# Optimization experiments

Measured on AMD Instinct MI355X. Metric: run time of the kernel, lower is better.

Reference implementation:

```python
import jax, jax.numpy as jnp
import numpy as np

B, C, H, W = 8, 320, 32, 32
HEADS, DHEAD = 8, 40
CTX_LEN, CTX_DIM = 77, 768
FF_INNER = 4 * C
GROUPS = 32
HW = H * W


def setup_inputs() -> dict:
    key = jax.random.key(0)
    ks = jax.random.split(key, 16)
    def nrm(k, shape, s=0.02):
        return (jax.random.normal(k, shape) * s).astype(jnp.float32)
    z = lambda *s: jnp.zeros(s, jnp.float32)
    o = lambda *s: jnp.ones(s, jnp.float32)
    inp = {}
    inp["x"] = jax.random.normal(ks[0], (B, C, H, W), jnp.float32)
    inp["context"] = jax.random.normal(ks[1], (B, CTX_LEN, CTX_DIM), jnp.float32)
    inp["vis_mask"] = jax.random.uniform(ks[2], (B, HW, HW)) > 0.5
    inp["v2t_mask"] = jax.random.uniform(ks[3], (B, HW, CTX_LEN)) > 0.5
    inp["gn_scale"] = o(C); inp["gn_bias"] = z(C)
    inp["proj_in_w"] = nrm(ks[4], (C, C)); inp["proj_in_b"] = z(C)
    inp["n1_s"] = o(C); inp["n1_b"] = z(C)
    inp["wq1"] = nrm(ks[5], (C, C)); inp["wk1"] = nrm(ks[6], (C, C)); inp["wv1"] = nrm(ks[7], (C, C))
    inp["wo1"] = nrm(ks[8], (C, C)); inp["bo1"] = z(C)
    inp["n2_s"] = o(C); inp["n2_b"] = z(C)
    inp["wq2"] = nrm(ks[9], (C, C)); inp["wk2"] = nrm(ks[10], (CTX_DIM, C)); inp["wv2"] = nrm(ks[11], (CTX_DIM, C))
    inp["wo2"] = nrm(ks[12], (C, C)); inp["bo2"] = z(C)
    inp["n3_s"] = o(C); inp["n3_b"] = z(C)
    inp["ff_w1"] = nrm(ks[13], (C, 2 * FF_INNER)); inp["ff_b1"] = z(2 * FF_INNER)
    inp["ff_w2"] = nrm(ks[14], (FF_INNER, C)); inp["ff_b2"] = z(C)
    inp["proj_out_w"] = nrm(ks[15], (C, C)); inp["proj_out_b"] = z(C)
    return inp


def group_norm(x, scale, bias, eps=1e-6):
    b, c, h, w = x.shape
    xg = x.reshape(b, GROUPS, -1)
    mu = xg.mean(-1, keepdims=True)
    var = xg.var(-1, keepdims=True)
    xn = ((xg - mu) * jax.lax.rsqrt(var + eps)).reshape(b, c, h, w)
    return xn * scale[None, :, None, None] + bias[None, :, None, None]


def layer_norm(x, s, b, eps=1e-5):
    mu = x.mean(-1, keepdims=True)
    var = x.var(-1, keepdims=True)
    return (x - mu) * jax.lax.rsqrt(var + eps) * s + b


def mha(xq, ctx, wq, wk, wv, wo, bo, mask):
    # CrossAttention: manual einsum softmax with boolean mask broadcast over heads
    b, n, _ = xq.shape
    m = ctx.shape[1]
    split = lambda t: t.reshape(b, -1, HEADS, DHEAD).transpose(0, 2, 1, 3)
    q = split(xq @ wq)   # [b,h,n,d]
    k = split(ctx @ wk)  # [b,h,m,d]
    v = split(ctx @ wv)
    sim = jnp.einsum('bhid,bhjd->bhij', q, k) * (DHEAD ** -0.5)
    if mask is not None:
        sim = jnp.where(mask[:, None, :, :], sim, jnp.finfo(sim.dtype).min)
    attn = jax.nn.softmax(sim, axis=-1)
    out = jnp.einsum('bhij,bhjd->bhid', attn, v)
    out = out.transpose(0, 2, 1, 3).reshape(b, n, HEADS * DHEAD)
    return out @ wo + bo


def reference(x, context, vis_mask, v2t_mask, gn_scale, gn_bias, proj_in_w, proj_in_b,
              n1_s, n1_b, wq1, wk1, wv1, wo1, bo1,
              n2_s, n2_b, wq2, wk2, wv2, wo2, bo2,
              n3_s, n3_b, ff_w1, ff_b1, ff_w2, ff_b2,
              proj_out_w, proj_out_b):
    x_in = x
    h = group_norm(x, gn_scale, gn_bias)
    # 1x1 conv proj_in == per-pixel linear; flatten b c h w -> b (hw) c
    h = h.reshape(B, C, HW).transpose(0, 2, 1) @ proj_in_w + proj_in_b
    # masked self-attention (vis mask)
    h = h + mha(layer_norm(h, n1_s, n1_b), layer_norm(h, n1_s, n1_b),
                wq1, wk1, wv1, wo1, bo1, vis_mask)
    # masked cross-attention to text (v2t mask)
    h = h + mha(layer_norm(h, n2_s, n2_b), context,
                wq2, wk2, wv2, wo2, bo2, v2t_mask)
    # GEGLU feedforward (glu=True, mult=4)
    y = layer_norm(h, n3_s, n3_b) @ ff_w1 + ff_b1
    a, g = jnp.split(y, 2, axis=-1)
    h = h + (a * jax.nn.gelu(g, approximate=False)) @ ff_w2 + ff_b2
    # proj_out + residual
    out = (h @ proj_out_w + proj_out_b).transpose(0, 2, 1).reshape(B, C, H, W)
    return out + x_in
```

## Files before the change

### kernel.cpp

```cpp
#include <hip/hip_runtime.h>
#include <hip/hip_bf16.h>
#include <math.h>


#define Bsz   8
#define Cch   320
#define HW    1024
#define NTOK  (Bsz*HW)
#define HEADS 8
#define DHEAD 40
#define CTXL  77
#define CTXD  768
#define FFI   1280
#define MCTX  (Bsz*CTXL)
#define MCTXP 640

typedef unsigned short u16;
typedef unsigned long long u64;
typedef __attribute__((ext_vector_type(8))) u16    u16x8;
typedef __attribute__((ext_vector_type(8))) __bf16 bf16x8;
typedef __attribute__((ext_vector_type(4))) float  f32x4;

__device__ inline u16 f2b(float f) {
    unsigned u = __float_as_uint(f);
    return (u16)((u + 0x7FFFu + ((u >> 16) & 1u)) >> 16);
}

__global__ __launch_bounds__(256) void gn_apply(
    const float* __restrict__ x, const float* __restrict__ gnA,
    const float* __restrict__ gnB, u16* __restrict__ out)
{
    __shared__ u16 T[64*72];
    const int tid = threadIdx.x;
    const int c0 = blockIdx.x * 64;
    const int p0 = blockIdx.y * 64;
    const int b  = blockIdx.z;
    for (int e = tid; e < 512; e += 256) {
        int r = e >> 3, ch = e & 7;
        const float* src = x + ((size_t)(b*Cch + c0 + r))*HW + p0 + ch*8;
        float a  = gnA[b*Cch + c0 + r];
        float bb = gnB[b*Cch + c0 + r];
        float4 v0 = *(const float4*)src;
        float4 v1 = *(const float4*)(src + 4);
        u16x8 val;
        val[0] = f2b(v0.x*a + bb); val[1] = f2b(v0.y*a + bb);
        val[2] = f2b(v0.z*a + bb); val[3] = f2b(v0.w*a + bb);
        val[4] = f2b(v1.x*a + bb); val[5] = f2b(v1.y*a + bb);
        val[6] = f2b(v1.z*a + bb); val[7] = f2b(v1.w*a + bb);
        *(u16x8*)&T[r*72 + (ch ^ (r & 7))*8] = val;
    }
    __syncthreads();
    for (int e = tid; e < 4096; e += 256) {
        int p = e >> 6, c = e & 63;
        u16 v = T[c*72 + (((p >> 3) ^ (c & 7))*8) + (p & 7)];
        out[((size_t)(b*HW + p0 + p))*Cch + c0 + c] = v;
    }
}

__global__ __launch_bounds__(256) void layernorm_kernel(
    const float* __restrict__ in, const float* __restrict__ s,
    const float* __restrict__ bgain, u16* __restrict__ out)
{
    int t = blockIdx.x*4 + (threadIdx.x >> 6);
    int lane = threadIdx.x & 63;
    const float* row = in + (size_t)t*Cch;
    float v[5];
    float sum = 0.f, sq = 0.f;
    #pragma unroll
    for (int i = 0; i < 5; ++i) {
        v[i] = row[lane + 64*i];
        sum += v[i]; sq += v[i]*v[i];
    }
    #pragma unroll
    for (int off = 32; off > 0; off >>= 1) {
        sum += __shfl_xor(sum, off);
        sq  += __shfl_xor(sq,  off);
    }
    float mean = sum * (1.f/320.f);
    float var  = sq  * (1.f/320.f) - mean*mean;
    float inv  = rsqrtf(var + 1e-5f);
    u16* orow = out + (size_t)t*Cch;
    #pragma unroll
    for (int i = 0; i < 5; ++i) {
        int c = lane + 64*i;
        orow[c] = f2b((v[i]-mean)*inv*s[c] + bgain[c]);
    }
}

struct WDesc { const float* src; u16* dst; int K; int N; int tiles; float scl; };
struct WPack { WDesc w[12]; };

#define WT_TILES 620
#define CTXBLK   240

__global__ __launch_bounds__(256) void preamble(
    WPack p, const float* __restrict__ ctxsrc, u16* __restrict__ ctxdst,
    const void* __restrict__ vis, const void* __restrict__ v2t,
    u64* __restrict__ bvis, u64* __restrict__ bv2t,
    const float* __restrict__ x, const float* __restrict__ gscale,
    const float* __restrict__ gbias, float* __restrict__ gnA,
    float* __restrict__ gnB)
{
    __shared__ u16 T[64*72];
    int blk = blockIdx.x;
    int tid = threadIdx.x;
    if (blk < WT_TILES) {
        int t = blk;
        #pragma unroll
        for (int i = 0; i < 12; ++i) {
            int nt = p.w[i].tiles;
            if (t < nt) {
                const int K = p.w[i].K, N = p.w[i].N;
                const int ntN = N >> 6;
                const int tk = t / ntN, tn = t - tk*ntN;
                const float scl = p.w[i].scl;
                const float* src = p.w[i].src;
                u16* dst = p.w[i].dst;
                for (int e = tid; e < 512; e += 256) {
                    int r = e >> 3, ch = e & 7;
                    const float* sp = src + (size_t)(tk*64 + r)*N + tn*64 + ch*8;
                    float4 v0 = *(const float4*)sp;
                    float4 v1 = *(const float4*)(sp + 4);
                    u16x8 val;
                    val[0] = f2b(v0.x*scl); val[1] = f2b(v0.y*scl);
                    val[2] = f2b(v0.z*scl); val[3] = f2b(v0.w*scl);
                    val[4] = f2b(v1.x*scl); val[5] = f2b(v1.y*scl);
                    val[6] = f2b(v1.z*scl); val[7] = f2b(v1.w*scl);
                    *(u16x8*)&T[r*72 + (ch ^ (r & 7))*8] = val;
                }
                __syncthreads();
                for (int e = tid; e < 4096; e += 256) {
                    int n = e >> 6, k = e & 63;
                    u16 v = T[k*72 + (((n >> 3) ^ (k & 7))*8) + (n & 7)];
                    dst[(size_t)(tn*64 + n)*K + tk*64 + k] = v;
                }
                return;
            }
            t -= nt;
        }
        return;
    }
    if (blk < WT_TILES + CTXBLK) {
        int idx = (blk - WT_TILES)*2048 + tid*8;
        int r = idx / CTXD;
        u16x8 val = {};
        if (r < MCTX) {
            float4 v0 = *(const float4*)(ctxsrc + idx);
            float4 v1 = *(const float4*)(ctxsrc + idx + 4);
            val[0] = f2b(v0.x); val[1] = f2b(v0.y);
            val[2] = f2b(v0.z); val[3] = f2b(v0.w);
            val[4] = f2b(v1.x); val[5] = f2b(v1.y);
            val[6] = f2b(v1.z); val[7] = f2b(v1.w);
        }
        *(u16x8*)(ctxdst + idx) = val;
        return;
    }
    if (blk >= WT_TILES + CTXBLK + 4096) {
        int gb = blk - (WT_TILES + CTXBLK + 4096);
        int b = gb >> 5, g = gb & 31;
        __shared__ float rs[256], rq[256];
        const float4* xg = (const float4*)(x + ((size_t)b*Cch + g*10)*HW);
        float s = 0.f, q = 0.f;
        #pragma unroll
        for (int i = 0; i < 10; ++i) {
            float4 v = xg[tid + i*256];
            s += v.x + v.y + v.z + v.w;
            q += v.x*v.x + v.y*v.y + v.z*v.z + v.w*v.w;
        }
        rs[tid] = s; rq[tid] = q; __syncthreads();
        for (int off = 128; off > 0; off >>= 1) {
            if (tid < off) { rs[tid] += rs[tid+off]; rq[tid] += rq[tid+off]; }
            __syncthreads();
        }
        if (tid < 10) {
            float mean = rs[0] * (1.f/10240.f);
            float var  = rq[0] * (1.f/10240.f) - mean*mean;
            float inv  = rsqrtf(var + 1e-6f);
            int chn = g*10 + tid;
            float a = inv * gscale[chn];
            gnA[b*Cch + chn] = a;
            gnB[b*Cch + chn] = gbias[chn] - mean*a;
        }
        return;
    }
    __shared__ int any;
    if (tid == 0) any = 0;
    __syncthreads();
    const unsigned char* probe = (const unsigned char*)vis;
    for (int i = tid; i < 4096; i += 256)
        if ((i & 3) && probe[i]) any = 1;
    __syncthreads();
    const int isU8 = any;
    int mb = blk - WT_TILES - CTXBLK;
    const void* mask; u64* bits; int Lkv, nw;
    if (mb < 2048) { mask = vis; bits = bvis; Lkv = HW;   nw = 16; }
    else           { mask = v2t; bits = bv2t; Lkv = CTXL; nw = 2; mb -= 2048; }
    const int wv = tid >> 6, lane = tid & 63;
    const int row = mb*4 + wv;
    const unsigned char* m8  = (const unsigned char*)mask;
    const int*           m32 = (const int*)mask;
    const size_t base = (size_t)row * Lkv;
    for (int w = 0; w < nw; ++w) {
        int j = w*64 + lane;
        bool on = (j < Lkv) && (isU8 ? (m8[base+j] != 0) : (m32[base+j] != 0));
        u64 word = __ballot(on);
        if (lane == 0) bits[(size_t)row*nw + w] = word;
    }
}

__global__ __launch_bounds__(512) void gemm_bf16(
    const u16* __restrict__ A, const u16* __restrict__ Wt,
    const float* __restrict__ bias, const float* __restrict__ res,
    float* __restrict__ out, u16* __restrict__ out_bf, int M, int N, int K)
{
    __shared__ u16 As[2][128*40];
    __shared__ u16 Bs[2][64*40];
    const int tid  = threadIdx.x;
    const int lane = tid & 63;
    const int w    = tid >> 6;
    const int mp   = w >> 1;
    const int np   = w & 1;
    const int m0   = blockIdx.y * 128;
    const int n0   = blockIdx.x * 64;
    const int fr   = lane & 15, fg = lane >> 4;
    const int ar   = tid >> 2, ac = tid & 3;
    const bool hasB = tid < 256;

    const u16* pa = A  + (size_t)(m0 + ar)*K + ac*8;
    const u16* pb = Wt + (size_t)(n0 + ar)*K + ac*8;
    const int nk = K >> 5;

    *(u16x8*)&As[0][ar*40 + ac*8] = *(const u16x8*)pa;
    if (hasB) *(u16x8*)&Bs[0][ar*40 + ac*8] = *(const u16x8*)pb;
    u16x8 xa = *(const u16x8*)(pa + 32);
    u16x8 ya = *(const u16x8*)(pa + 64);
    u16x8 xb = {}, yb = {};
    if (hasB) { xb = *(const u16x8*)(pb + 32); yb = *(const u16x8*)(pb + 64); }

    f32x4 acc[2][2] = {};
    for (int i = 0; i < nk; i += 2) {
        __syncthreads();
        *(u16x8*)&As[1][ar*40 + ac*8] = xa;
        if (hasB) *(u16x8*)&Bs[1][ar*40 + ac*8] = xb;
        if (i + 3 < nk) {
            xa = *(const u16x8*)(pa + 32*(i+3));
            if (hasB) xb = *(const u16x8*)(pb + 32*(i+3));
        }
        {
            bf16x8 a0 = *(const bf16x8*)&As[0][(mp*32      + fr)*40 + fg*8];
            bf16x8 a1 = *(const bf16x8*)&As[0][(mp*32 + 16 + fr)*40 + fg*8];
            #pragma unroll
            for (int t = 0; t < 2; ++t) {
                bf16x8 b = *(const bf16x8*)&Bs[0][((np*2+t)*16 + fr)*40 + fg*8];
                acc[0][t] = __builtin_amdgcn_mfma_f32_16x16x32_bf16(a0, b, acc[0][t], 0, 0, 0);
                acc[1][t] = __builtin_amdgcn_mfma_f32_16x16x32_bf16(a1, b, acc[1][t], 0, 0, 0);
            }
        }
        __syncthreads();
        if (i + 2 < nk) {
            *(u16x8*)&As[0][ar*40 + ac*8] = ya;
            if (hasB) *(u16x8*)&Bs[0][ar*40 + ac*8] = yb;
            if (i + 4 < nk) {
                ya = *(const u16x8*)(pa + 32*(i+4));
                if (hasB) yb = *(const u16x8*)(pb + 32*(i+4));
            }
        }
        {
            bf16x8 a0 = *(const bf16x8*)&As[1][(mp*32      + fr)*40 + fg*8];
            bf16x8 a1 = *(const bf16x8*)&As[1][(mp*32 + 16 + fr)*40 + fg*8];
            #pragma unroll
            for (int t = 0; t < 2; ++t) {
                bf16x8 b = *(const bf16x8*)&Bs[1][((np*2+t)*16 + fr)*40 + fg*8];
                acc[0][t] = __builtin_amdgcn_mfma_f32_16x16x32_bf16(a0, b, acc[0][t], 0, 0, 0);
                acc[1][t] = __builtin_amdgcn_mfma_f32_16x16x32_bf16(a1, b, acc[1][t], 0, 0, 0);
            }
        }
    }
    #pragma unroll
    for (int at = 0; at < 2; ++at) {
        #pragma unroll
        for (int t = 0; t < 2; ++t) {
            int gn = n0 + (np*2+t)*16 + fr;
            float bv = bias ? bias[gn] : 0.f;
            #pragma unroll
            for (int i = 0; i < 4; ++i) {
                int gm = m0 + mp*32 + at*16 + fg*4 + i;
                float v = acc[at][t][i] + bv;
                if (res) v += res[(size_t)gm*N + gn];
                if (out) out[(size_t)gm*N + gn] = v;
                if (out_bf) out_bf[(size_t)gm*N + gn] = f2b(v);
            }
        }
    }
}

__global__ __launch_bounds__(512) void gemm_pout(
    const u16* __restrict__ A, const u16* __restrict__ Wt,
    const float* __restrict__ bias, const float* __restrict__ x,
    float* __restrict__ out, int K)
{
    __shared__ u16 As[2][128*40];
    __shared__ u16 Bs[2][64*40];
    const int tid  = threadIdx.x;
    const int lane = tid & 63;
    const int w    = tid >> 6;
    const int mp   = w >> 1;
    const int np   = w & 1;
    const int m0   = blockIdx.y * 128;
    const int n0   = blockIdx.x * 64;
    const int fr   = lane & 15, fg = lane >> 4;
    const int ar   = tid >> 2, ac = tid & 3;
    const bool hasB = tid < 256;

    const u16* pa = A  + (size_t)(m0 + ar)*K + ac*8;
    const u16* pb = Wt + (size_t)(n0 + ar)*K + ac*8;
    const int nk = K >> 5;

    *(u16x8*)&As[0][ar*40 + ac*8] = *(const u16x8*)pa;
    if (hasB) *(u16x8*)&Bs[0][ar*40 + ac*8] = *(const u16x8*)pb;
    u16x8 xa = *(const u16x8*)(pa + 32);
    u16x8 ya = *(const u16x8*)(pa + 64);
    u16x8 xb = {}, yb = {};
    if (hasB) { xb = *(const u16x8*)(pb + 32); yb = *(const u16x8*)(pb + 64); }

    f32x4 acc[2][2] = {};
    for (int i = 0; i < nk; i += 2) {
        __syncthreads();
        *(u16x8*)&As[1][ar*40 + ac*8] = xa;
        if (hasB) *(u16x8*)&Bs[1][ar*40 + ac*8] = xb;
        if (i + 3 < nk) {
            xa = *(const u16x8*)(pa + 32*(i+3));
            if (hasB) xb = *(const u16x8*)(pb + 32*(i+3));
        }
        {
            bf16x8 a0 = *(const bf16x8*)&As[0][(mp*32      + fr)*40 + fg*8];
            bf16x8 a1 = *(const bf16x8*)&As[0][(mp*32 + 16 + fr)*40 + fg*8];
            #pragma unroll
            for (int t = 0; t < 2; ++t) {
                bf16x8 b = *(const bf16x8*)&Bs[0][((np*2+t)*16 + fr)*40 + fg*8];
                acc[0][t] = __builtin_amdgcn_mfma_f32_16x16x32_bf16(a0, b, acc[0][t], 0, 0, 0);
                acc[1][t] = __builtin_amdgcn_mfma_f32_16x16x32_bf16(a1, b, acc[1][t], 0, 0, 0);
            }
        }
        __syncthreads();
        if (i + 2 < nk) {
            *(u16x8*)&As[0][ar*40 + ac*8] = ya;
            if (hasB) *(u16x8*)&Bs[0][ar*40 + ac*8] = yb;
            if (i + 4 < nk) {
                ya = *(const u16x8*)(pa + 32*(i+4));
                if (hasB) yb = *(const u16x8*)(pb + 32*(i+4));
            }
        }
        {
            bf16x8 a0 = *(const bf16x8*)&As[1][(mp*32      + fr)*40 + fg*8];
            bf16x8 a1 = *(const bf16x8*)&As[1][(mp*32 + 16 + fr)*40 + fg*8];
            #pragma unroll
            for (int t = 0; t < 2; ++t) {
                bf16x8 b = *(const bf16x8*)&Bs[1][((np*2+t)*16 + fr)*40 + fg*8];
                acc[0][t] = __builtin_amdgcn_mfma_f32_16x16x32_bf16(a0, b, acc[0][t], 0, 0, 0);
                acc[1][t] = __builtin_amdgcn_mfma_f32_16x16x32_bf16(a1, b, acc[1][t], 0, 0, 0);
            }
        }
    }
    #pragma unroll
    for (int at = 0; at < 2; ++at) {
        #pragma unroll
        for (int t = 0; t < 2; ++t) {
            int gn = n0 + (np*2+t)*16 + fr;
            float bv = bias[gn];
            int gm0 = m0 + mp*32 + at*16 + fg*4;
            int b   = gm0 >> 10;
            int pcol= gm0 & (HW-1);
            size_t o = ((size_t)(b*Cch + gn))*HW + pcol;
            f32x4 xv = *(const f32x4*)&x[o];
            f32x4 vv;
            #pragma unroll
            for (int i = 0; i < 4; ++i) vv[i] = acc[at][t][i] + bv + xv[i];
            *(f32x4*)&out[o] = vv;
        }
    }
}

__global__ __launch_bounds__(512) void ctx_kv_gemm(
    const u16* __restrict__ ctx, const u16* __restrict__ wk,
    const u16* __restrict__ wv, u16* __restrict__ kout, u16* __restrict__ vout)
{
    __shared__ u16 As[2][64*40];
    __shared__ u16 Bs[2][64*40];
    const int tid  = threadIdx.x;
    const int lane = tid & 63;
    const int w    = tid >> 6;
    const int mg   = w >> 1;
    const int np   = w & 1;
    const int m0   = blockIdx.y * 64;
    const int n0   = blockIdx.x * 64;
    const u16* Wt  = blockIdx.z ? wv : wk;
    u16* outp      = blockIdx.z ? vout : kout;
    const int fr   = lane & 15, fg = lane >> 4;
    const bool isA = tid < 256;
    const int cr   = (tid & 255) >> 2, cc = tid & 3;

    const u16* ps = isA ? ctx + (size_t)(m0 + cr)*CTXD + cc*8
                        : Wt  + (size_t)(n0 + cr)*CTXD + cc*8;
    u16* s0 = isA ? &As[0][cr*40 + cc*8] : &Bs[0][cr*40 + cc*8];
    u16* s1 = isA ? &As[1][cr*40 + cc*8] : &Bs[1][cr*40 + cc*8];
    const int nk = CTXD >> 5;

    *(u16x8*)s0 = *(const u16x8*)ps;
    u16x8 xv = *(const u16x8*)(ps + 32);
    u16x8 yv = *(const u16x8*)(ps + 64);

    f32x4 acc[2] = {};
    for (int i = 0; i < nk; i += 2) {
        __syncthreads();
        *(u16x8*)s1 = xv;
        if (i + 3 < nk) xv = *(const u16x8*)(ps + 32*(i+3));
        {
            bf16x8 a = *(const bf16x8*)&As[0][(mg*16 + fr)*40 + fg*8];
            #pragma unroll
            for (int t = 0; t < 2; ++t) {
                bf16x8 b = *(const bf16x8*)&Bs[0][((np*2+t)*16 + fr)*40 + fg*8];
                acc[t] = __builtin_amdgcn_mfma_f32_16x16x32_bf16(a, b, acc[t], 0, 0, 0);
            }
        }
        __syncthreads();
        if (i + 2 < nk) {
            *(u16x8*)s0 = yv;
            if (i + 4 < nk) yv = *(const u16x8*)(ps + 32*(i+4));
        }
        {
            bf16x8 a = *(const bf16x8*)&As[1][(mg*16 + fr)*40 + fg*8];
            #pragma unroll
            for (int t = 0; t < 2; ++t) {
                bf16x8 b = *(const bf16x8*)&Bs[1][((np*2+t)*16 + fr)*40 + fg*8];
                acc[t] = __builtin_amdgcn_mfma_f32_16x16x32_bf16(a, b, acc[t], 0, 0, 0);
            }
        }
    }
    #pragma unroll
    for (int t = 0; t < 2; ++t) {
        int gn = n0 + (np*2+t)*16 + fr;
        #pragma unroll
        for (int i = 0; i < 4; ++i) {
            int gm = m0 + mg*16 + fg*4 + i;
            if (gm < MCTX)
                outp[(size_t)gm*Cch + gn] = f2b(acc[t][i]);
        }
    }
}

__global__ __launch_bounds__(512) void geglu_bf16(
    const u16* __restrict__ A, const u16* __restrict__ Wt,
    const float* __restrict__ b1, u16* __restrict__ out, int M, int K)
{
    __shared__ u16 As[2][128*40];
    __shared__ u16 Ba[2][64*40];
    __shared__ u16 Bg[2][64*40];
    const int tid  = threadIdx.x;
    const int lane = tid & 63;
    const int w    = tid >> 6;
    const int mp   = w >> 1;
    const int np   = w & 1;
    const int m0   = blockIdx.y * 128;
    const int n0   = blockIdx.x * 64;
    const int fr   = lane & 15, fg = lane >> 4;
    const int ar   = tid >> 2, ac = tid & 3;
    const int nk   = K >> 5;

    const u16* pa = A + (size_t)(m0 + ar)*K + ac*8;
    const int bq = (ar < 64) ? (n0 + ar) : (FFI + n0 + ar - 64);
    const u16* pb = Wt + (size_t)bq*K + ac*8;
    u16* bs0 = (ar < 64) ? &Ba[0][ar*40 + ac*8] : &Bg[0][(ar-64)*40 + ac*8];
    u16* bs1 = (ar < 64) ? &Ba[1][ar*40 + ac*8] : &Bg[1][(ar-64)*40 + ac*8];

    *(u16x8*)&As[0][ar*40 + ac*8] = *(const u16x8*)pa;
    *(u16x8*)bs0 = *(const u16x8*)pb;
    u16x8 xa = *(const u16x8*)(pa + 32);
    u16x8 xb = *(const u16x8*)(pb + 32);
    u16x8 ya = *(const u16x8*)(pa + 64);
    u16x8 yb = *(const u16x8*)(pb + 64);

    f32x4 aca[2][2] = {}, acg[2][2] = {};
    for (int i = 0; i < nk; i += 2) {
        __syncthreads();
        *(u16x8*)&As[1][ar*40 + ac*8] = xa;
        *(u16x8*)bs1 = xb;
        if (i + 3 < nk) {
            xa = *(const u16x8*)(pa + 32*(i+3));
            xb = *(const u16x8*)(pb + 32*(i+3));
        }
        {
            bf16x8 a0 = *(const bf16x8*)&As[0][(mp*32      + fr)*40 + fg*8];
            bf16x8 a1 = *(const bf16x8*)&As[0][(mp*32 + 16 + fr)*40 + fg*8];
            #pragma unroll
            for (int t = 0; t < 2; ++t) {
                bf16x8 ba = *(const bf16x8*)&Ba[0][((np*2+t)*16 + fr)*40 + fg*8];
                bf16x8 bg = *(const bf16x8*)&Bg[0][((np*2+t)*16 + fr)*40 + fg*8];
                aca[0][t] = __builtin_amdgcn_mfma_f32_16x16x32_bf16(a0, ba, aca[0][t], 0, 0, 0);
                aca[1][t] = __builtin_amdgcn_mfma_f32_16x16x32_bf16(a1, ba, aca[1][t], 0, 0, 0);
                acg[0][t] = __builtin_amdgcn_mfma_f32_16x16x32_bf16(a0, bg, acg[0][t], 0, 0, 0);
                acg[1][t] = __builtin_amdgcn_mfma_f32_16x16x32_bf16(a1, bg, acg[1][t], 0, 0, 0);
            }
        }
        __syncthreads();
        if (i + 2 < nk) {
            *(u16x8*)&As[0][ar*40 + ac*8] = ya;
            *(u16x8*)bs0 = yb;
            if (i + 4 < nk) {
                ya = *(const u16x8*)(pa + 32*(i+4));
                yb = *(const u16x8*)(pb + 32*(i+4));
            }
        }
        {
            bf16x8 a0 = *(const bf16x8*)&As[1][(mp*32      + fr)*40 + fg*8];
            bf16x8 a1 = *(const bf16x8*)&As[1][(mp*32 + 16 + fr)*40 + fg*8];
            #pragma unroll
            for (int t = 0; t < 2; ++t) {
                bf16x8 ba = *(const bf16x8*)&Ba[1][((np*2+t)*16 + fr)*40 + fg*8];
                bf16x8 bg = *(const bf16x8*)&Bg[1][((np*2+t)*16 + fr)*40 + fg*8];
                aca[0][t] = __builtin_amdgcn_mfma_f32_16x16x32_bf16(a0, ba, aca[0][t], 0, 0, 0);
                aca[1][t] = __builtin_amdgcn_mfma_f32_16x16x32_bf16(a1, ba, aca[1][t], 0, 0, 0);
                acg[0][t] = __builtin_amdgcn_mfma_f32_16x16x32_bf16(a0, bg, acg[0][t], 0, 0, 0);
                acg[1][t] = __builtin_amdgcn_mfma_f32_16x16x32_bf16(a1, bg, acg[1][t], 0, 0, 0);
            }
        }
    }
    #pragma unroll
    for (int at = 0; at < 2; ++at) {
        #pragma unroll
        for (int t = 0; t < 2; ++t) {
            int gn = n0 + (np*2+t)*16 + fr;
            float ba = b1[gn], bg = b1[FFI + gn];
            #pragma unroll
            for (int i = 0; i < 4; ++i) {
                int gm = m0 + mp*32 + at*16 + fg*4 + i;
                float av = aca[at][t][i] + ba;
                float gv = acg[at][t][i] + bg;
                float gel = 0.5f*gv*(1.f + erff(gv*0.70710678118654752f));
                out[(size_t)gm*FFI + gn] = f2b(av*gel);
            }
        }
    }
}

__global__ __launch_bounds__(256) void transpose_v(
    const u16* __restrict__ in, int istride, u16* __restrict__ out,
    int Ltok, int ostride)
{
    __shared__ u16 T[64*72];
    const int tid = threadIdx.x;
    const int c0 = blockIdx.x * 64;
    const int t0 = blockIdx.y * 64;
    const int b  = blockIdx.z;
    for (int e = tid; e < 512; e += 256) {
        int r = e >> 3, ch = e & 7;
        u16x8 val = {};
        if (t0 + r < Ltok)
            val = *(const u16x8*)(in + ((size_t)(b*Ltok + t0 + r))*istride + c0 + ch*8);
        *(u16x8*)&T[r*72 + (ch ^ (r & 7))*8] = val;
    }
    __syncthreads();
    for (int e = tid; e < 4096; e += 256) {
        int c = e >> 6, t = e & 63;
        u16 v = T[t*72 + (((c >> 3) ^ (t & 7))*8) + (c & 7)];
        out[((size_t)(b*Cch + c0 + c))*ostride + t0 + t] = v;
    }
}

__global__ __launch_bounds__(512) void flash_mfma(
    const u16* __restrict__ qb, int qstride,
    const u16* __restrict__ kb, int kstride,
    const u16* __restrict__ vt, int vstride,
    const u64* __restrict__ mbits, int nw,
    u16* __restrict__ out,
    int Lkv)
{
    __shared__ u16 QPs[128*72];
    __shared__ u16 Ks[2][64*72];
    __shared__ u16 Vs[2][48*72];

    const int tid  = threadIdx.x;
    const int lane = tid & 63;
    const int w    = tid >> 6;
    const int col  = lane & 15;
    const int quad = lane >> 4;
    const int bi   = blockIdx.x;
    const int hb   = (bi & 7)*8 + (bi >> 6);
    const int qt   = (bi >> 3) & 7;
    const int h    = hb & 7;
    const int b    = hb >> 3;
    const int q0   = qt*128;
    const int ch   = tid & 7;
    const int r0   = tid >> 3;

    {
        const u16* qT = qb + ((size_t)(b*HW + q0))*qstride + (size_t)h*DHEAD + ch*8;
        u16x8 v0 = {}, v1 = {};
        if (ch < 5) {
            v0 = *(const u16x8*)(qT + (size_t)r0*qstride);
            v1 = *(const u16x8*)(qT + (size_t)(r0+64)*qstride);
        }
        *(u16x8*)&QPs[r0*72 + ch*8]      = v0;
        *(u16x8*)&QPs[(r0+64)*72 + ch*8] = v1;
    }
    if (tid < 128) {
        int rr  = tid >> 3;
        int row = 40 + (rr & 7);
        int buf = rr >> 3;
        u16x8 v = {};
        if (row == DHEAD) {
            #pragma unroll
            for (int z = 0; z < 8; ++z) v[z] = 0x3F80;
        }
        *(u16x8*)&Vs[buf][row*72 + ch*8] = v;
    }

    const bool kok = ch < 5;
    const u16* kR = kb + (size_t)b*Lkv*kstride + (size_t)h*DHEAD + ch*8
                       + (size_t)r0*kstride;
    const u16* vR = vt + ((size_t)(b*Cch + h*DHEAD))*vstride + ch*8
                       + (size_t)r0*vstride;
    const bool vok = r0 < DHEAD;
    const u64* mrow = mbits + ((size_t)(b*HW + q0 + w*16 + quad*4))*nw;

    u16x8 nk = {}, nv = {};
    if (kok && r0 < Lkv) nk = *(const u16x8*)kR;
    if (vok) nv = *(const u16x8*)vR;

    __syncthreads();
    const bf16x8 qa0 = *(const bf16x8*)&QPs[(w*16 + col)*72 +  0 + quad*8];
    const bf16x8 qa1 = *(const bf16x8*)&QPs[(w*16 + col)*72 + 32 + quad*8];

    f32x4 acc_o[3] = {};

    const int nkt = (Lkv + 63) / 64;
    int cur = 0;
    for (int jt = 0; jt < nkt; ++jt) {
        *(u16x8*)&Ks[cur][r0*72 + ch*8] = nk;
        if (vok) *(u16x8*)&Vs[cur][r0*72 + ch*8] = nv;
        if (jt + 1 < nkt) {
            kR += (size_t)64*kstride;
            vR += 64;
            nk = (u16x8){};
            if (kok && ((jt+1)*64 + r0 < Lkv)) nk = *(const u16x8*)kR;
            if (vok) nv = *(const u16x8*)vR;
        }
        __syncthreads();

        u64 mw[4];
        #pragma unroll
        for (int i = 0; i < 4; ++i) mw[i] = mrow[i*nw + jt];

        f32x4 s[4] = {};
        #pragma unroll
        for (int nt = 0; nt < 4; ++nt) {
            bf16x8 b0 = *(const bf16x8*)&Ks[cur][(nt*16 + col)*72 +  0 + quad*8];
            bf16x8 b1 = *(const bf16x8*)&Ks[cur][(nt*16 + col)*72 + 32 + quad*8];
            s[nt] = __builtin_amdgcn_mfma_f32_16x16x32_bf16(qa0, b0, s[nt], 0, 0, 0);
            s[nt] = __builtin_amdgcn_mfma_f32_16x16x32_bf16(qa1, b1, s[nt], 0, 0, 0);
        }

        #pragma unroll
        for (int i = 0; i < 4; ++i) {
            #pragma unroll
            for (int nt = 0; nt < 4; ++nt) {
                float p = __builtin_amdgcn_exp2f(s[nt][i]);
                unsigned bits = (unsigned)(mw[i] >> (nt*16));
                s[nt][i] = ((bits >> col) & 1u) ? p : 0.f;
            }
        }

        #pragma unroll
        for (int nt = 0; nt < 4; ++nt)
            #pragma unroll
            for (int i = 0; i < 4; ++i)
                QPs[(w*16 + quad*4 + i)*68 + nt*16 + col] =
                    (u16)(__float_as_uint(s[nt][i]) >> 16);

        bf16x8 pa0, pa1;
        __builtin_memcpy(&pa0, &QPs[(w*16 + col)*68 +  0 + quad*8], 16);
        __builtin_memcpy(&pa1, &QPs[(w*16 + col)*68 + 32 + quad*8], 16);
        #pragma unroll
        for (int nt = 0; nt < 3; ++nt) {
            bf16x8 vb0 = *(const bf16x8*)&Vs[cur][(nt*16 + col)*72 +  0 + quad*8];
            bf16x8 vb1 = *(const bf16x8*)&Vs[cur][(nt*16 + col)*72 + 32 + quad*8];
            acc_o[nt] = __builtin_amdgcn_mfma_f32_16x16x32_bf16(pa0, vb0, acc_o[nt], 0, 0, 0);
            acc_o[nt] = __builtin_amdgcn_mfma_f32_16x16x32_bf16(pa1, vb1, acc_o[nt], 0, 0, 0);
        }
        cur ^= 1;
    }

    float inv_l[4];
    #pragma unroll
    for (int i = 0; i < 4; ++i)
        inv_l[i] = 1.f / __shfl(acc_o[2][i], (lane & 48) | 8);

    #pragma unroll
    for (int nt = 0; nt < 3; ++nt) {
        int d = nt*16 + col;
        if (d < DHEAD) {
            #pragma unroll
            for (int i = 0; i < 4; ++i) {
                int q = q0 + w*16 + quad*4 + i;
                out[((size_t)(b*HW + q))*Cch + h*DHEAD + d] = f2b(acc_o[nt][i] * inv_l[i]);
            }
        }
    }
}

extern "C" void kernel_launch(void* const* d_in, const int* in_sizes, int n_in,
                              void* d_out, int out_size, void* d_ws, size_t ws_size,
                              hipStream_t stream)
{
    const float* x        = (const float*)d_in[0];
    const float* context  = (const float*)d_in[1];
    const void*  vis_mask = d_in[2];
    const void*  v2t_mask = d_in[3];
    const float* gn_s     = (const float*)d_in[4];
    const float* gn_b     = (const float*)d_in[5];
    const float* proj_in_w= (const float*)d_in[6];
    const float* proj_in_b= (const float*)d_in[7];
    const float* n1_s     = (const float*)d_in[8];
    const float* n1_b     = (const float*)d_in[9];
    const float* wq1      = (const float*)d_in[10];
    const float* wk1      = (const float*)d_in[11];
    const float* wv1      = (const float*)d_in[12];
    const float* wo1      = (const float*)d_in[13];
    const float* bo1      = (const float*)d_in[14];
    const float* n2_s     = (const float*)d_in[15];
    const float* n2_b     = (const float*)d_in[16];
    const float* wq2      = (const float*)d_in[17];
    const float* wk2      = (const float*)d_in[18];
    const float* wv2      = (const float*)d_in[19];
    const float* wo2      = (const float*)d_in[20];
    const float* bo2      = (const float*)d_in[21];
    const float* n3_s     = (const float*)d_in[22];
    const float* n3_b     = (const float*)d_in[23];
    const float* ff_w1    = (const float*)d_in[24];
    const float* ff_b1    = (const float*)d_in[25];
    const float* ff_w2    = (const float*)d_in[26];
    const float* ff_b2    = (const float*)d_in[27];
    const float* pout_w   = (const float*)d_in[28];
    const float* pout_b   = (const float*)d_in[29];
    float* out = (float*)d_out;

    const size_t TOKC = (size_t)NTOK*Cch;
    float* ws   = (float*)d_ws;
    float* Hb   = ws;
    u16*   QKV  = (u16*)(Hb + TOKC);
    u16*   Vt_g = QKV + 3*TOKC;
    u16*   G_bf = QKV;
    u16*   T0b  = Vt_g + TOKC;
    u16*   T1b  = T0b + TOKC;
    u16*   Hb_bf= T1b + TOKC;
    u16*   Wbf  = Hb_bf + TOKC;
    u64*   mb_vis = (u64*)(Wbf + 2539520);
    u64*   mb_v2t = mb_vis + 131072;
    u16*   ctx_bf = (u16*)(mb_v2t + 16384);
    u16*   Kc_bf  = ctx_bf + MCTXP*CTXD;
    u16*   Vc_bf  = Kc_bf + 640*Cch;
    float* gnA    = (float*)(Vc_bf + 640*Cch);
    float* gnB    = gnA + Bsz*Cch;

    u16* w_q1  = Wbf;
    u16* w_k1  = Wbf +  102400;
    u16* w_v1  = Wbf +  204800;
    u16* w_pin = Wbf +  307200;
    u16* w_o1  = Wbf +  409600;
    u16* w_q2  = Wbf +  512000;
    u16* w_o2  = Wbf +  614400;
    u16* w_ff1 = Wbf +  716800;
    u16* w_ff2 = Wbf + 1536000;
    u16* w_po  = Wbf + 1945600;
    u16* w_k2  = Wbf + 2048000;
    u16* w_v2  = Wbf + 2293760;

    const float qscale = 0.15811388300841897f * 1.4426950408889634f;
    WPack pack;
    pack.w[0]  = { wq1,       w_q1,  Cch, Cch, 25,  qscale };
    pack.w[1]  = { wk1,       w_k1,  Cch, Cch, 25,  1.f };
    pack.w[2]  = { wv1,       w_v1,  Cch, Cch, 25,  1.f };
    pack.w[3]  = { proj_in_w, w_pin, Cch, Cch, 25,  1.f };
    pack.w[4]  = { wo1,       w_o1,  Cch, Cch, 25,  1.f };
    pack.w[5]  = { wq2,       w_q2,  Cch, Cch, 25,  qscale };
    pack.w[6]  = { wo2,       w_o2,  Cch, Cch, 25,  1.f };
    pack.w[7]  = { ff_w1,     w_ff1, Cch, 2*FFI, 200, 1.f };
    pack.w[8]  = { ff_w2,     w_ff2, FFI, Cch, 100, 1.f };
    pack.w[9]  = { pout_w,    w_po,  Cch, Cch, 25,  1.f };
    pack.w[10] = { wk2,       w_k2,  CTXD, Cch, 60, 1.f };
    pack.w[11] = { wv2,       w_v2,  CTXD, Cch, 60, 1.f };

    dim3 blk256(256);
    dim3 blk512(512);
    dim3 gTok(Cch/64, NTOK/128);
    dim3 gQKV(960/64, NTOK/128);
    dim3 gKV(Cch/64, MCTXP/64, 2);
    dim3 gFF(FFI/64, NTOK/128);
    dim3 gTrS(Cch/64, HW/64, Bsz);
    dim3 gTrX(Cch/64, 2, Bsz);
    dim3 gGN(Cch/64, HW/64, Bsz);

    preamble<<<WT_TILES + CTXBLK + 4096 + 256, blk256, 0, stream>>>(
        pack, context, ctx_bf, vis_mask, v2t_mask, mb_vis, mb_v2t,
        x, gn_s, gn_b, gnA, gnB);

    gn_apply<<<gGN, blk256, 0, stream>>>(x, gnA, gnB, T0b);
    gemm_bf16<<<gTok, blk512, 0, stream>>>(T0b, w_pin, proj_in_b, nullptr, Hb, nullptr, NTOK, Cch, Cch);

    layernorm_kernel<<<NTOK/4, blk256, 0, stream>>>(Hb, n1_s, n1_b, T0b);
    gemm_bf16<<<gQKV, blk512, 0, stream>>>(T0b, w_q1, nullptr, nullptr, nullptr, QKV, NTOK, 960, Cch);
    transpose_v<<<gTrS, blk256, 0, stream>>>(QKV + 640, 960, Vt_g, HW, HW);
    flash_mfma<<<512, blk512, 0, stream>>>(QKV, 960, QKV + 320, 960, Vt_g, HW,
                                           mb_vis, 16, T1b, HW);
    gemm_bf16<<<gTok, blk512, 0, stream>>>(T1b, w_o1, bo1, Hb, Hb, nullptr, NTOK, Cch, Cch);

    layernorm_kernel<<<NTOK/4, blk256, 0, stream>>>(Hb, n2_s, n2_b, T0b);
    gemm_bf16<<<gTok, blk512, 0, stream>>>(T0b, w_q2, nullptr, nullptr, nullptr, QKV, NTOK, Cch, Cch);
    ctx_kv_gemm<<<gKV, blk512, 0, stream>>>(ctx_bf, w_k2, w_v2, Kc_bf, Vc_bf);
    transpose_v<<<gTrX, blk256, 0, stream>>>(Vc_bf, Cch, Vt_g, CTXL, 128);
    flash_mfma<<<512, blk512, 0, stream>>>(QKV, Cch, Kc_bf, Cch, Vt_g, 128,
                                           mb_v2t, 2, T1b, CTXL);
    gemm_bf16<<<gTok, blk512, 0, stream>>>(T1b, w_o2, bo2, Hb, Hb, nullptr, NTOK, Cch, Cch);

    layernorm_kernel<<<NTOK/4, blk256, 0, stream>>>(Hb, n3_s, n3_b, T0b);
    geglu_bf16<<<gFF, blk512, 0, stream>>>(T0b, w_ff1, ff_b1, G_bf, NTOK, Cch);
    gemm_bf16<<<gTok, blk512, 0, stream>>>(G_bf, w_ff2, ff_b2, Hb, nullptr, Hb_bf, NTOK, Cch, FFI);

    gemm_pout<<<gTok, blk512, 0, stream>>>(Hb_bf, w_po, pout_b, x, out, Cch);
}
```

Baseline: 375.9 us.

## Fuse LayerNorm into GEMM prologues and merge context KV and transposes

Removes the standalone layernorm kernels. Each consuming GEMM (QKV, Q2, GEGLU) now computes per-row mean and variance from the fp32 residual and normalises while staging A tiles to bf16. The context K/V GEMM now runs as extra blocks of the first QKV launch, and the two V transposes are merged into one launch, which cuts launch count and the bf16 round trip through global memory. The trade-off is that every N-tile block re-reads the fp32 rows to compute statistics, so A-side traffic is duplicated across column tiles. The fused blocks also carry extra register pressure.

```diff
diff --git a/kernel.cpp b/kernel.cpp
--- a/kernel.cpp
+++ b/kernel.cpp
@@ -54,36 +54,6 @@
         int p = e >> 6, c = e & 63;
         u16 v = T[c*72 + (((p >> 3) ^ (c & 7))*8) + (p & 7)];
         out[((size_t)(b*HW + p0 + p))*Cch + c0 + c] = v;
-    }
-}
-
-__global__ __launch_bounds__(256) void layernorm_kernel(
-    const float* __restrict__ in, const float* __restrict__ s,
-    const float* __restrict__ bgain, u16* __restrict__ out)
-{
-    int t = blockIdx.x*4 + (threadIdx.x >> 6);
-    int lane = threadIdx.x & 63;
-    const float* row = in + (size_t)t*Cch;
-    float v[5];
-    float sum = 0.f, sq = 0.f;
-    #pragma unroll
-    for (int i = 0; i < 5; ++i) {
-        v[i] = row[lane + 64*i];
-        sum += v[i]; sq += v[i]*v[i];
-    }
-    #pragma unroll
-    for (int off = 32; off > 0; off >>= 1) {
-        sum += __shfl_xor(sum, off);
-        sq  += __shfl_xor(sq,  off);
-    }
-    float mean = sum * (1.f/320.f);
-    float var  = sq  * (1.f/320.f) - mean*mean;
-    float inv  = rsqrtf(var + 1e-5f);
-    u16* orow = out + (size_t)t*Cch;
-    #pragma unroll
-    for (int i = 0; i < 5; ++i) {
-        int c = lane + 64*i;
-        orow[c] = f2b((v[i]-mean)*inv*s[c] + bgain[c]);
     }
 }
 
@@ -294,6 +264,194 @@
     }
 }
 
+__global__ __launch_bounds__(512) void gemm_ln(
+    const float* __restrict__ Af, const float* __restrict__ lns,
+    const float* __restrict__ lnb, const u16* __restrict__ Wt,
+    u16* __restrict__ out_bf, int N, int nqkv,
+    const u16* __restrict__ ctx, const u16* __restrict__ wk,
+    const u16* __restrict__ wv, u16* __restrict__ kout, u16* __restrict__ vout)
+{
+    __shared__ u16 As[2][128*40];
+    __shared__ u16 Bs[2][64*40];
+    const int tid  = threadIdx.x;
+    const int lane = tid & 63;
+    const int w    = tid >> 6;
+    const int fr   = lane & 15, fg = lane >> 4;
+    const int bi   = blockIdx.x;
+
+    if (bi < nqkv) {
+        const int K  = Cch;
+        const int nx = N >> 6;
+        const int n0 = (bi % nx)*64;
+        const int m0 = (bi / nx)*128;
+        const int mp = w >> 1, np = w & 1;
+        const int ar = tid >> 2, ac = tid & 3;
+        const bool hasB = tid < 256;
+
+        const float* rowp = Af + (size_t)(m0 + ar)*K;
+        float mean, inv;
+        {
+            const float* pp = rowp + ac*80;
+            float sum = 0.f, sq = 0.f;
+            #pragma unroll
+            for (int i = 0; i < 20; ++i) {
+                float4 v = *(const float4*)(pp + i*4);
+                sum += v.x+v.y+v.z+v.w;
+                sq  += v.x*v.x+v.y*v.y+v.z*v.z+v.w*v.w;
+            }
+            sum += __shfl_xor(sum, 1); sq += __shfl_xor(sq, 1);
+            sum += __shfl_xor(sum, 2); sq += __shfl_xor(sq, 2);
+            mean = sum * (1.f/320.f);
+            inv  = rsqrtf(sq * (1.f/320.f) - mean*mean + 1e-5f);
+        }
+
+        const float* paf = rowp + ac*8;
+        const u16*   pb  = Wt + (size_t)(n0 + ar)*K + ac*8;
+        const int nk = K >> 5;
+
+        #define LNPACK(v0, v1, c) ({                                        \
+            float4 s0_ = *(const float4*)(lns+(c)), s1_ = *(const float4*)(lns+(c)+4); \
+            float4 g0_ = *(const float4*)(lnb+(c)), g1_ = *(const float4*)(lnb+(c)+4); \
+            u16x8 r_;                                                       \
+            r_[0]=f2b(((v0).x-mean)*inv*s0_.x+g0_.x);                       \
+            r_[1]=f2b(((v0).y-mean)*inv*s0_.y+g0_.y);                       \
+            r_[2]=f2b(((v0).z-mean)*inv*s0_.z+g0_.z);                       \
+            r_[3]=f2b(((v0).w-mean)*inv*s0_.w+g0_.w);                       \
+            r_[4]=f2b(((v1).x-mean)*inv*s1_.x+g1_.x);                       \
+            r_[5]=f2b(((v1).y-mean)*inv*s1_.y+g1_.y);                       \
+            r_[6]=f2b(((v1).z-mean)*inv*s1_.z+g1_.z);                       \
+            r_[7]=f2b(((v1).w-mean)*inv*s1_.w+g1_.w);                       \
+            r_; })
+
+        {
+            float4 v0 = *(const float4*)paf, v1 = *(const float4*)(paf+4);
+            *(u16x8*)&As[0][ar*40 + ac*8] = LNPACK(v0, v1, ac*8);
+        }
+        if (hasB) *(u16x8*)&Bs[0][ar*40 + ac*8] = *(const u16x8*)pb;
+        float4 xa0 = *(const float4*)(paf+32), xa1 = *(const float4*)(paf+36);
+        float4 ya0 = *(const float4*)(paf+64), ya1 = *(const float4*)(paf+68);
+        u16x8 xb = {}, yb = {};
+        if (hasB) { xb = *(const u16x8*)(pb+32); yb = *(const u16x8*)(pb+64); }
+
+        f32x4 acc[2][2] = {};
+        for (int i = 0; i < nk; i += 2) {
+            __syncthreads();
+            *(u16x8*)&As[1][ar*40 + ac*8] = LNPACK(xa0, xa1, (i+1)*32 + ac*8);
+            if (hasB) *(u16x8*)&Bs[1][ar*40 + ac*8] = xb;
+            if (i + 3 < nk) {
+                xa0 = *(const float4*)(paf + 32*(i+3));
+                xa1 = *(const float4*)(paf + 32*(i+3) + 4);
+                if (hasB) xb = *(const u16x8*)(pb + 32*(i+3));
+            }
+            {
+                bf16x8 a0 = *(const bf16x8*)&As[0][(mp*32      + fr)*40 + fg*8];
+                bf16x8 a1 = *(const bf16x8*)&As[0][(mp*32 + 16 + fr)*40 + fg*8];
+                #pragma unroll
+                for (int t = 0; t < 2; ++t) {
+                    bf16x8 b = *(const bf16x8*)&Bs[0][((np*2+t)*16 + fr)*40 + fg*8];
+                    acc[0][t] = __builtin_amdgcn_mfma_f32_16x16x32_bf16(a0, b, acc[0][t], 0, 0, 0);
+                    acc[1][t] = __builtin_amdgcn_mfma_f32_16x16x32_bf16(a1, b, acc[1][t], 0, 0, 0);
+                }
+            }
+            __syncthreads();
+            if (i + 2 < nk) {
+                *(u16x8*)&As[0][ar*40 + ac*8] = LNPACK(ya0, ya1, (i+2)*32 + ac*8);
+                if (hasB) *(u16x8*)&Bs[0][ar*40 + ac*8] = yb;
+                if (i + 4 < nk) {
+                    ya0 = *(const float4*)(paf + 32*(i+4));
+                    ya1 = *(const float4*)(paf + 32*(i+4) + 4);
+                    if (hasB) yb = *(const u16x8*)(pb + 32*(i+4));
+                }
+            }
+            {
+                bf16x8 a0 = *(const bf16x8*)&As[1][(mp*32      + fr)*40 + fg*8];
+                bf16x8 a1 = *(const bf16x8*)&As[1][(mp*32 + 16 + fr)*40 + fg*8];
+                #pragma unroll
+                for (int t = 0; t < 2; ++t) {
+                    bf16x8 b = *(const bf16x8*)&Bs[1][((np*2+t)*16 + fr)*40 + fg*8];
+                    acc[0][t] = __builtin_amdgcn_mfma_f32_16x16x32_bf16(a0, b, acc[0][t], 0, 0, 0);
+                    acc[1][t] = __builtin_amdgcn_mfma_f32_16x16x32_bf16(a1, b, acc[1][t], 0, 0, 0);
+                }
+            }
+        }
+        #undef LNPACK
+        #pragma unroll
+        for (int at = 0; at < 2; ++at) {
+            #pragma unroll
+            for (int t = 0; t < 2; ++t) {
+                int gn = n0 + (np*2+t)*16 + fr;
+                #pragma unroll
+                for (int i = 0; i < 4; ++i) {
+                    int gm = m0 + mp*32 + at*16 + fg*4 + i;
+                    out_bf[(size_t)gm*N + gn] = f2b(acc[at][t][i]);
+                }
+            }
+        }
+        return;
+    }
+
+    {
+        int cb = bi - nqkv;
+        const int z  = cb / 50; cb -= z*50;
+        const int my = cb / 5, nx0 = cb - my*5;
+        const int m0 = my*64, n0 = nx0*64;
+        const u16* Wt2 = z ? wv : wk;
+        u16* outp      = z ? vout : kout;
+        const int mg = w >> 1;
+        const int np = w & 1;
+        const bool isA = tid < 256;
+        const int cr = (tid & 255) >> 2, cc = tid & 3;
+
+        const u16* ps = isA ? ctx + (size_t)(m0 + cr)*CTXD + cc*8
+                            : Wt2 + (size_t)(n0 + cr)*CTXD + cc*8;
+        u16* s0 = isA ? &As[0][cr*40 + cc*8] : &Bs[0][cr*40 + cc*8];
+        u16* s1 = isA ? &As[1][cr*40 + cc*8] : &Bs[1][cr*40 + cc*8];
+        const int nk = CTXD >> 5;
+
+        *(u16x8*)s0 = *(const u16x8*)ps;
+        u16x8 xv = *(const u16x8*)(ps + 32);
+        u16x8 yv = *(const u16x8*)(ps + 64);
+
+        f32x4 acc[2] = {};
+        for (int i = 0; i < nk; i += 2) {
+            __syncthreads();
+            *(u16x8*)s1 = xv;
+            if (i + 3 < nk) xv = *(const u16x8*)(ps + 32*(i+3));
+            {
+                bf16x8 a = *(const bf16x8*)&As[0][(mg*16 + fr)*40 + fg*8];
+                #pragma unroll
+                for (int t = 0; t < 2; ++t) {
+                    bf16x8 b = *(const bf16x8*)&Bs[0][((np*2+t)*16 + fr)*40 + fg*8];
+                    acc[t] = __builtin_amdgcn_mfma_f32_16x16x32_bf16(a, b, acc[t], 0, 0, 0);
+                }
+            }
+            __syncthreads();
+            if (i + 2 < nk) {
+                *(u16x8*)s0 = yv;
+                if (i + 4 < nk) yv = *(const u16x8*)(ps + 32*(i+4));
+            }
+            {
+                bf16x8 a = *(const bf16x8*)&As[1][(mg*16 + fr)*40 + fg*8];
+                #pragma unroll
+                for (int t = 0; t < 2; ++t) {
+                    bf16x8 b = *(const bf16x8*)&Bs[1][((np*2+t)*16 + fr)*40 + fg*8];
+                    acc[t] = __builtin_amdgcn_mfma_f32_16x16x32_bf16(a, b, acc[t], 0, 0, 0);
+                }
+            }
+        }
+        #pragma unroll
+        for (int t = 0; t < 2; ++t) {
+            int gn = n0 + (np*2+t)*16 + fr;
+            #pragma unroll
+            for (int i = 0; i < 4; ++i) {
+                int gm = m0 + mg*16 + fg*4 + i;
+                if (gm < MCTX)
+                    outp[(size_t)gm*Cch + gn] = f2b(acc[t][i]);
+            }
+        }
+    }
+}
+
 __global__ __launch_bounds__(512) void gemm_pout(
     const u16* __restrict__ A, const u16* __restrict__ Wt,
     const float* __restrict__ bias, const float* __restrict__ x,
@@ -381,77 +539,10 @@
     }
 }
 
-__global__ __launch_bounds__(512) void ctx_kv_gemm(
-    const u16* __restrict__ ctx, const u16* __restrict__ wk,
-    const u16* __restrict__ wv, u16* __restrict__ kout, u16* __restrict__ vout)
-{
-    __shared__ u16 As[2][64*40];
-    __shared__ u16 Bs[2][64*40];
-    const int tid  = threadIdx.x;
-    const int lane = tid & 63;
-    const int w    = tid >> 6;
-    const int mg   = w >> 1;
-    const int np   = w & 1;
-    const int m0   = blockIdx.y * 64;
-    const int n0   = blockIdx.x * 64;
-    const u16* Wt  = blockIdx.z ? wv : wk;
-    u16* outp      = blockIdx.z ? vout : kout;
-    const int fr   = lane & 15, fg = lane >> 4;
-    const bool isA = tid < 256;
-    const int cr   = (tid & 255) >> 2, cc = tid & 3;
-
-    const u16* ps = isA ? ctx + (size_t)(m0 + cr)*CTXD + cc*8
-                        : Wt  + (size_t)(n0 + cr)*CTXD + cc*8;
-    u16* s0 = isA ? &As[0][cr*40 + cc*8] : &Bs[0][cr*40 + cc*8];
-    u16* s1 = isA ? &As[1][cr*40 + cc*8] : &Bs[1][cr*40 + cc*8];
-    const int nk = CTXD >> 5;
-
-    *(u16x8*)s0 = *(const u16x8*)ps;
-    u16x8 xv = *(const u16x8*)(ps + 32);
-    u16x8 yv = *(const u16x8*)(ps + 64);
-
-    f32x4 acc[2] = {};
-    for (int i = 0; i < nk; i += 2) {
-        __syncthreads();
-        *(u16x8*)s1 = xv;
-        if (i + 3 < nk) xv = *(const u16x8*)(ps + 32*(i+3));
-        {
-            bf16x8 a = *(const bf16x8*)&As[0][(mg*16 + fr)*40 + fg*8];
-            #pragma unroll
-            for (int t = 0; t < 2; ++t) {
-                bf16x8 b = *(const bf16x8*)&Bs[0][((np*2+t)*16 + fr)*40 + fg*8];
-                acc[t] = __builtin_amdgcn_mfma_f32_16x16x32_bf16(a, b, acc[t], 0, 0, 0);
-            }
-        }
-        __syncthreads();
-        if (i + 2 < nk) {
-            *(u16x8*)s0 = yv;
-            if (i + 4 < nk) yv = *(const u16x8*)(ps + 32*(i+4));
-        }
-        {
-            bf16x8 a = *(const bf16x8*)&As[1][(mg*16 + fr)*40 + fg*8];
-            #pragma unroll
-            for (int t = 0; t < 2; ++t) {
-                bf16x8 b = *(const bf16x8*)&Bs[1][((np*2+t)*16 + fr)*40 + fg*8];
-                acc[t] = __builtin_amdgcn_mfma_f32_16x16x32_bf16(a, b, acc[t], 0, 0, 0);
-            }
-        }
-    }
-    #pragma unroll
-    for (int t = 0; t < 2; ++t) {
-        int gn = n0 + (np*2+t)*16 + fr;
-        #pragma unroll
-        for (int i = 0; i < 4; ++i) {
-            int gm = m0 + mg*16 + fg*4 + i;
-            if (gm < MCTX)
-                outp[(size_t)gm*Cch + gn] = f2b(acc[t][i]);
-        }
-    }
-}
-
-__global__ __launch_bounds__(512) void geglu_bf16(
-    const u16* __restrict__ A, const u16* __restrict__ Wt,
-    const float* __restrict__ b1, u16* __restrict__ out, int M, int K)
+__global__ __launch_bounds__(512) void geglu_ln(
+    const float* __restrict__ Af, const float* __restrict__ lns,
+    const float* __restrict__ lnb, const u16* __restrict__ Wt,
+    const float* __restrict__ b1, u16* __restrict__ out)
 {
     __shared__ u16 As[2][128*40];
     __shared__ u16 Ba[2][64*40];
@@ -465,29 +556,65 @@
     const int n0   = blockIdx.x * 64;
     const int fr   = lane & 15, fg = lane >> 4;
     const int ar   = tid >> 2, ac = tid & 3;
+    const int K    = Cch;
     const int nk   = K >> 5;
 
-    const u16* pa = A + (size_t)(m0 + ar)*K + ac*8;
+    const float* rowp = Af + (size_t)(m0 + ar)*K;
+    float mean, inv;
+    {
+        const float* pp = rowp + ac*80;
+        float sum = 0.f, sq = 0.f;
+        #pragma unroll
+        for (int i = 0; i < 20; ++i) {
+            float4 v = *(const float4*)(pp + i*4);
+            sum += v.x+v.y+v.z+v.w;
+            sq  += v.x*v.x+v.y*v.y+v.z*v.z+v.w*v.w;
+        }
+        sum += __shfl_xor(sum, 1); sq += __shfl_xor(sq, 1);
+        sum += __shfl_xor(sum, 2); sq += __shfl_xor(sq, 2);
+        mean = sum * (1.f/320.f);
+        inv  = rsqrtf(sq * (1.f/320.f) - mean*mean + 1e-5f);
+    }
+
+    const float* paf = rowp + ac*8;
     const int bq = (ar < 64) ? (n0 + ar) : (FFI + n0 + ar - 64);
     const u16* pb = Wt + (size_t)bq*K + ac*8;
     u16* bs0 = (ar < 64) ? &Ba[0][ar*40 + ac*8] : &Bg[0][(ar-64)*40 + ac*8];
     u16* bs1 = (ar < 64) ? &Ba[1][ar*40 + ac*8] : &Bg[1][(ar-64)*40 + ac*8];
 
-    *(u16x8*)&As[0][ar*40 + ac*8] = *(const u16x8*)pa;
+    #define LNPACK(v0, v1, c) ({                                            \
+        float4 s0_ = *(const float4*)(lns+(c)), s1_ = *(const float4*)(lns+(c)+4); \
+        float4 g0_ = *(const float4*)(lnb+(c)), g1_ = *(const float4*)(lnb+(c)+4); \
+        u16x8 r_;                                                           \
+        r_[0]=f2b(((v0).x-mean)*inv*s0_.x+g0_.x);                           \
+        r_[1]=f2b(((v0).y-mean)*inv*s0_.y+g0_.y);                           \
+        r_[2]=f2b(((v0).z-mean)*inv*s0_.z+g0_.z);                           \
+        r_[3]=f2b(((v0).w-mean)*inv*s0_.w+g0_.w);                           \
+        r_[4]=f2b(((v1).x-mean)*inv*s1_.x+g1_.x);                           \
+        r_[5]=f2b(((v1).y-mean)*inv*s1_.y+g1_.y);                           \
+        r_[6]=f2b(((v1).z-mean)*inv*s1_.z+g1_.z);                           \
+        r_[7]=f2b(((v1).w-mean)*inv*s1_.w+g1_.w);                           \
+        r_; })
+
+    {
+        float4 v0 = *(const float4*)paf, v1 = *(const float4*)(paf+4);
+        *(u16x8*)&As[0][ar*40 + ac*8] = LNPACK(v0, v1, ac*8);
+    }
     *(u16x8*)bs0 = *(const u16x8*)pb;
-    u16x8 xa = *(const u16x8*)(pa + 32);
+    float4 xa0 = *(const float4*)(paf+32), xa1 = *(const float4*)(paf+36);
+    float4 ya0 = *(const float4*)(paf+64), ya1 = *(const float4*)(paf+68);
     u16x8 xb = *(const u16x8*)(pb + 32);
-    u16x8 ya = *(const u16x8*)(pa + 64);
     u16x8 yb = *(const u16x8*)(pb + 64);
 
     f32x4 aca[2][2] = {}, acg[2][2] = {};
     for (int i = 0; i < nk; i += 2) {
         __syncthreads();
-        *(u16x8*)&As[1][ar*40 + ac*8] = xa;
+        *(u16x8*)&As[1][ar*40 + ac*8] = LNPACK(xa0, xa1, (i+1)*32 + ac*8);
         *(u16x8*)bs1 = xb;
         if (i + 3 < nk) {
-            xa = *(const u16x8*)(pa + 32*(i+3));
-            xb = *(const u16x8*)(pb + 32*(i+3));
+            xa0 = *(const float4*)(paf + 32*(i+3));
+            xa1 = *(const float4*)(paf + 32*(i+3) + 4);
+            xb  = *(const u16x8*)(pb + 32*(i+3));
         }
         {
             bf16x8 a0 = *(const bf16x8*)&As[0][(mp*32      + fr)*40 + fg*8];
@@ -504,11 +631,12 @@
         }
         __syncthreads();
         if (i + 2 < nk) {
-            *(u16x8*)&As[0][ar*40 + ac*8] = ya;
+            *(u16x8*)&As[0][ar*40 + ac*8] = LNPACK(ya0, ya1, (i+2)*32 + ac*8);
             *(u16x8*)bs0 = yb;
             if (i + 4 < nk) {
-                ya = *(const u16x8*)(pa + 32*(i+4));
-                yb = *(const u16x8*)(pb + 32*(i+4));
+                ya0 = *(const float4*)(paf + 32*(i+4));
+                ya1 = *(const float4*)(paf + 32*(i+4) + 4);
+                yb  = *(const u16x8*)(pb + 32*(i+4));
             }
         }
         {
@@ -525,6 +653,7 @@
             }
         }
     }
+    #undef LNPACK
     #pragma unroll
     for (int at = 0; at < 2; ++at) {
         #pragma unroll
@@ -543,15 +672,22 @@
     }
 }
 
-__global__ __launch_bounds__(256) void transpose_v(
-    const u16* __restrict__ in, int istride, u16* __restrict__ out,
-    int Ltok, int ostride)
+__global__ __launch_bounds__(256) void transpose_both(
+    const u16* __restrict__ vself, u16* __restrict__ vt_self,
+    const u16* __restrict__ vcross, u16* __restrict__ vt_cross)
 {
     __shared__ u16 T[64*72];
     const int tid = threadIdx.x;
-    const int c0 = blockIdx.x * 64;
-    const int t0 = blockIdx.y * 64;
-    const int b  = blockIdx.z;
+    const int bi  = blockIdx.x;
+    const u16* in; u16* out; int istride, Ltok, ostride, c0, t0, b;
+    if (bi < 640) {
+        c0 = (bi % 5)*64; t0 = ((bi/5) & 15)*64; b = bi/80;
+        in = vself;  istride = 960; Ltok = HW;   out = vt_self;  ostride = HW;
+    } else {
+        int cb = bi - 640;
+        c0 = (cb % 5)*64; t0 = ((cb/5) & 1)*64;  b = cb/10;
+        in = vcross; istride = Cch; Ltok = CTXL; out = vt_cross; ostride = 128;
+    }
     for (int e = tid; e < 512; e += 256) {
         int r = e >> 3, ch = e & 7;
         u16x8 val = {};
@@ -761,6 +897,7 @@
     u16*   Vc_bf  = Kc_bf + 640*Cch;
     float* gnA    = (float*)(Vc_bf + 640*Cch);
     float* gnB    = gnA + Bsz*Cch;
+    u16*   Vt_x   = (u16*)(gnB + Bsz*Cch);
 
     u16* w_q1  = Wbf;
     u16* w_k1  = Wbf +  102400;
@@ -793,11 +930,7 @@
     dim3 blk256(256);
     dim3 blk512(512);
     dim3 gTok(Cch/64, NTOK/128);
-    dim3 gQKV(960/64, NTOK/128);
-    dim3 gKV(Cch/64, MCTXP/64, 2);
     dim3 gFF(FFI/64, NTOK/128);
-    dim3 gTrS(Cch/64, HW/64, Bsz);
-    dim3 gTrX(Cch/64, 2, Bsz);
     dim3 gGN(Cch/64, HW/64, Bsz);
 
     preamble<<<WT_TILES + CTXBLK + 4096 + 256, blk256, 0, stream>>>(
@@ -807,23 +940,20 @@
     gn_apply<<<gGN, blk256, 0, stream>>>(x, gnA, gnB, T0b);
     gemm_bf16<<<gTok, blk512, 0, stream>>>(T0b, w_pin, proj_in_b, nullptr, Hb, nullptr, NTOK, Cch, Cch);
 
-    layernorm_kernel<<<NTOK/4, blk256, 0, stream>>>(Hb, n1_s, n1_b, T0b);
-    gemm_bf16<<<gQKV, blk512, 0, stream>>>(T0b, w_q1, nullptr, nullptr, nullptr, QKV, NTOK, 960, Cch);
-    transpose_v<<<gTrS, blk256, 0, stream>>>(QKV + 640, 960, Vt_g, HW, HW);
+    gemm_ln<<<960 + 100, blk512, 0, stream>>>(Hb, n1_s, n1_b, w_q1, QKV, 960, 960,
+                                              ctx_bf, w_k2, w_v2, Kc_bf, Vc_bf);
+    transpose_both<<<720, blk256, 0, stream>>>(QKV + 640, Vt_g, Vc_bf, Vt_x);
     flash_mfma<<<512, blk512, 0, stream>>>(QKV, 960, QKV + 320, 960, Vt_g, HW,
                                            mb_vis, 16, T1b, HW);
     gemm_bf16<<<gTok, blk512, 0, stream>>>(T1b, w_o1, bo1, Hb, Hb, nullptr, NTOK, Cch, Cch);
 
-    layernorm_kernel<<<NTOK/4, blk256, 0, stream>>>(Hb, n2_s, n2_b, T0b);
-    gemm_bf16<<<gTok, blk512, 0, stream>>>(T0b, w_q2, nullptr, nullptr, nullptr, QKV, NTOK, Cch, Cch);
-    ctx_kv_gemm<<<gKV, blk512, 0, stream>>>(ctx_bf, w_k2, w_v2, Kc_bf, Vc_bf);
-    transpose_v<<<gTrX, blk256, 0, stream>>>(Vc_bf, Cch, Vt_g, CTXL, 128);
-    flash_mfma<<<512, blk512, 0, stream>>>(QKV, Cch, Kc_bf, Cch, Vt_g, 128,
+    gemm_ln<<<320, blk512, 0, stream>>>(Hb, n2_s, n2_b, w_q2, QKV, Cch, 320,
+                                        ctx_bf, w_k2, w_v2, Kc_bf, Vc_bf);
+    flash_mfma<<<512, blk512, 0, stream>>>(QKV, Cch, Kc_bf, Cch, Vt_x, 128,
                                            mb_v2t, 2, T1b, CTXL);
     gemm_bf16<<<gTok, blk512, 0, stream>>>(T1b, w_o2, bo2, Hb, Hb, nullptr, NTOK, Cch, Cch);
 
-    layernorm_kernel<<<NTOK/4, blk256, 0, stream>>>(Hb, n3_s, n3_b, T0b);
-    geglu_bf16<<<gFF, blk512, 0, stream>>>(T0b, w_ff1, ff_b1, G_bf, NTOK, Cch);
+    geglu_ln<<<gFF, blk512, 0, stream>>>(Hb, n3_s, n3_b, w_ff1, ff_b1, G_bf);
     gemm_bf16<<<gTok, blk512, 0, stream>>>(G_bf, w_ff2, ff_b2, Hb, nullptr, Hb_bf, NTOK, Cch, FFI);
 
     gemm_pout<<<gTok, blk512, 0, stream>>>(Hb_bf, w_po, pout_b, x, out, Cch);
```

Result: slower. 421.7 us (+12.2%).
